# Kernel optimization log

Hardware: AMD Instinct MI355X
Metric: run time of the kernel (lower is better)

The kernel has to match this reference:

```python
import jax, jax.numpy as jnp
import numpy as np

N = 50000      # nodes
E = 800000     # edges
F_IN = 64      # num_node_features
H = 128        # hidden_channels
C = 2          # num_classes
G = 16         # graphs in batch


def setup_inputs() -> dict:
    key = jax.random.key(0)
    ks = jax.random.split(key, 16)
    def lin(k, fan_in, shape):
        return jax.random.normal(k, shape, jnp.float32) / np.sqrt(fan_in)
    return {
        "x": jax.random.normal(ks[0], (N, F_IN), jnp.float32),
        "edge_index": jax.random.randint(ks[1], (2, E), 0, N, dtype=jnp.int32),
        "batch": jnp.sort(jax.random.randint(ks[2], (N,), 0, G, dtype=jnp.int32)),
        "W1": lin(ks[3], F_IN, (F_IN, H)), "b1": jnp.zeros((H,), jnp.float32),
        "W2": lin(ks[4], H, (H, H)),       "b2": jnp.zeros((H,), jnp.float32),
        "W3": lin(ks[5], H, (H, H)),       "b3": jnp.zeros((H,), jnp.float32),
        "W4": lin(ks[6], H, (H, H)),       "b4": jnp.zeros((H,), jnp.float32),
        "lw1": lin(ks[7], H, (H, H // 2)), "lb1": jnp.zeros((H // 2,), jnp.float32),
        "lw2": lin(ks[8], H // 2, (H // 2, C)), "lb2": jnp.zeros((C,), jnp.float32),
    }


def _graph_norm(edge_index):
    # PyG GCNConv default: add self-loops, symmetric normalization.
    loop = jnp.arange(N, dtype=edge_index.dtype)
    src = jnp.concatenate([edge_index[0], loop])  # message source
    dst = jnp.concatenate([edge_index[1], loop])  # aggregation target
    deg = jax.ops.segment_sum(jnp.ones_like(dst, jnp.float32), dst, num_segments=N)
    dinv = jnp.where(deg > 0, jax.lax.rsqrt(deg), 0.0)
    norm = dinv[src] * dinv[dst]                  # [E+N]
    return src, dst, norm


def _gcn_conv(h, W, b, src, dst, norm):
    hw = h @ W                                    # [N, out]
    msg = hw[src] * norm[:, None]                 # gather + normalize  [E+N, out]
    agg = jax.ops.segment_sum(msg, dst, num_segments=N)  # scatter-add
    return agg + b


def reference(x, edge_index, batch, W1, b1, W2, b2, W3, b3, W4, b4, lw1, lb1, lw2, lb2):
    src, dst, norm = _graph_norm(edge_index)
    h = jax.nn.relu(_gcn_conv(x, W1, b1, src, dst, norm))   # dropout inactive (eval)
    h = jax.nn.relu(_gcn_conv(h, W2, b2, src, dst, norm))
    h = jax.nn.relu(_gcn_conv(h, W3, b3, src, dst, norm))
    h = _gcn_conv(h, W4, b4, src, dst, norm)
    # global_mean_pool over graph ids
    cnt = jax.ops.segment_sum(jnp.ones((N,), jnp.float32), batch, num_segments=G)
    pooled = jax.ops.segment_sum(h, batch, num_segments=G) / jnp.maximum(cnt, 1.0)[:, None]
    out = jax.nn.relu(pooled @ lw1 + lb1)
    return out @ lw2 + lb2
```

## Files before the change

### kernel.cpp

```cpp
#include <hip/hip_runtime.h>

#define NN 50000
#define NPAD 50048
#define NE 800000
#define FIN 64
#define H 128
#define NG 16
#define NPART 64
#define NBUCK 196
#define BUCK_CAP 4800
#define FILLA_BLOCKS 512
#define FILLA_CHUNK 1563
#define ROW_U 64
#define XROW_U 32
#define DUMMY NN
#define ZERO_I4 32768
#define PREP_ITEMS (H * FIN + 2 * H * H + ZERO_I4)
#define PREP_BLOCKS ((PREP_ITEMS + 255) / 256)

typedef __bf16 bf16x8 __attribute__((ext_vector_type(8)));
typedef float f32x4 __attribute__((ext_vector_type(4)));
typedef float f32x2 __attribute__((ext_vector_type(2)));
typedef unsigned int u32x4 __attribute__((ext_vector_type(4)));

__device__ inline unsigned short bf16r(float x) {
    unsigned int u = __float_as_uint(x);
    return (unsigned short)((u + 0x7fffu + ((u >> 16) & 1u)) >> 16);
}
__device__ inline unsigned int pack_bf16x2(float a, float b) {
    return (unsigned int)bf16r(a) | ((unsigned int)bf16r(b) << 16);
}
__device__ inline float bf_lo(unsigned int u) { return __uint_as_float(u << 16); }
__device__ inline float bf_hi(unsigned int u) { return __uint_as_float(u & 0xffff0000u); }

__device__ inline void pkadd(f32x2& a, unsigned int u) {
    f32x2 p;
    p.x = bf_lo(u);
    p.y = bf_hi(u);
    asm("v_pk_add_f32 %0, %1, %0" : "+v"(a) : "v"(p));
}
__device__ inline void bfly(f32x2& a, int m) {
    a.x += __shfl_xor(a.x, m);
    a.y += __shfl_xor(a.y, m);
}

__global__ __launch_bounds__(256) void fillA_prep_kernel(const int* __restrict__ ei,
                                                         int* __restrict__ gcount,
                                                         unsigned int* __restrict__ ebuf,
                                                         const float* __restrict__ W1,
                                                         const float* __restrict__ W2,
                                                         const float* __restrict__ W3,
                                                         unsigned short* __restrict__ Wt1,
                                                         unsigned short* __restrict__ Wt2,
                                                         unsigned short* __restrict__ Wt3,
                                                         int4* __restrict__ zbuf) {
    const int t = threadIdx.x;
    if (blockIdx.x >= FILLA_BLOCKS) {
        int e = (blockIdx.x - FILLA_BLOCKS) * 256 + t;
        if (e < H * FIN) {
            int n = e / FIN, k = e % FIN;
            Wt1[e] = bf16r(W1[k * H + n]);
            return;
        }
        int u = e - H * FIN;
        if (u < 2 * H * H) {
            const float* W = W2;
            unsigned short* Wt = Wt2;
            if (u >= H * H) { W = W3; Wt = Wt3; u -= H * H; }
            int n = u / H, k = u % H;
            Wt[u] = bf16r(W[k * H + n]);
            return;
        }
        int z = u - 2 * H * H;
        if (z < ZERO_I4) zbuf[z] = make_int4(0, 0, 0, 0);
        return;
    }
    __shared__ int hist[256];
    __shared__ int base[256];
    hist[t] = 0;
    __syncthreads();
    const int e0 = blockIdx.x * FILLA_CHUNK;
    const int e1 = min(e0 + FILLA_CHUNK, NE);
    for (int e = e0 + t; e < e1; e += 256)
        atomicAdd(&hist[ei[NE + e] >> 8], 1);
    __syncthreads();
    {
        int h = hist[t];
        base[t] = h ? atomicAdd(&gcount[t], h) : 0;
    }
    __syncthreads();
    for (int e = e0 + t; e < e1; e += 256) {
        int d = ei[NE + e];
        int s = ei[e];
        int b = d >> 8;
        int pos = atomicAdd(&base[b], 1);
        ebuf[b * BUCK_CAP + pos] = (unsigned int)s | ((unsigned int)d << 16);
    }
}

__global__ __launch_bounds__(256) void fillB_kernel(const unsigned int* __restrict__ ebuf,
                                                    const int* __restrict__ gcount,
                                                    int* __restrict__ galloc,
                                                    int* __restrict__ pcnt,
                                                    const int* __restrict__ batch,
                                                    int2* __restrict__ rowse,
                                                    float* __restrict__ dinv,
                                                    unsigned short* __restrict__ csr) {
    __shared__ int lh[256];
    __shared__ int lsum[256];
    __shared__ int lcur[256];
    __shared__ int lgc[16];
    __shared__ int base_s;
    const int b = blockIdx.x, t = threadIdx.x;
    const int n0 = b * 256;
    lh[t] = 0;
    if (t < 16) lgc[t] = 0;
    __syncthreads();
    const int ne = gcount[b];
    const unsigned int* __restrict__ eb = ebuf + b * BUCK_CAP;
    for (int i = t; i < ne; i += 256)
        atomicAdd(&lh[(int)(eb[i] >> 16) - n0], 1);
    __syncthreads();
    const int c = lh[t];
    const int p = (c + 7) & ~7;
    const int n = n0 + t;
    if (n < NN) atomicAdd(&lgc[batch[n]], 1);
    lsum[t] = p;
    __syncthreads();
    if (t < 16 && lgc[t]) atomicAdd(&pcnt[t], lgc[t]);
    for (int off = 1; off < 256; off <<= 1) {
        int u = (t >= off) ? lsum[t - off] : 0;
        __syncthreads();
        lsum[t] += u;
        __syncthreads();
    }
    if (t == 255) base_s = atomicAdd(galloc, lsum[255]);
    const int excl = t ? lsum[t - 1] : 0;
    __syncthreads();
    const int st = base_s + excl;
    if (n < NN) {
        rowse[n] = make_int2(st, st + p);
        dinv[n] = rsqrtf((float)c + 1.0f);
    } else if (n < NPAD) {
        rowse[n] = make_int2(0, 0);
        dinv[n] = 0.0f;
    }
    lcur[t] = st;
    __syncthreads();
    for (int i = t; i < ne; i += 256) {
        unsigned int u = eb[i];
        int pos = atomicAdd(&lcur[(int)(u >> 16) - n0], 1);
        csr[pos] = (unsigned short)(u & 0xFFFFu);
    }
    __syncthreads();
    for (int k = st + c; k < st + p; k++) csr[k] = (unsigned short)DUMMY;
}

__global__ __launch_bounds__(256) void xprep_kernel(const float* __restrict__ x,
                                                    const float* __restrict__ dinv,
                                                    unsigned short* __restrict__ xb) {
    const int idx = blockIdx.x * 256 + threadIdx.x;
    const int e4 = idx * 4;
    const int n = e4 >> 6;
    uint2 o;
    if (n < NN) {
        float4 v = *(const float4*)&x[e4];
        float d = dinv[n];
        o.x = pack_bf16x2(v.x * d, v.y * d);
        o.y = pack_bf16x2(v.z * d, v.w * d);
    } else {
        o.x = o.y = 0u;
    }
    *(uint2*)&xb[e4] = o;
}

#define LSTRIDE 130
template <int K, int EPI>
__global__ __launch_bounds__(256) void gemm_mfma_kernel(const unsigned short* __restrict__ hb,
                                                        const unsigned short* __restrict__ Wt,
                                                        const float* __restrict__ dinv,
                                                        const float* __restrict__ bias,
                                                        unsigned int* __restrict__ outu) {
    __shared__ float ls[64 * LSTRIDE];
    const int wave = threadIdx.x >> 6, lane = threadIdx.x & 63;
    const int m15 = lane & 15, quad = lane >> 4;
    const int row0 = blockIdx.x * 64;
    const int arow = row0 + wave * 16 + m15;

    bf16x8 a[K / 32];
#pragma unroll
    for (int ks = 0; ks < K / 32; ks++)
        a[ks] = *(const bf16x8*)&hb[(size_t)arow * K + ks * 32 + quad * 8];

    const int lrow = wave * 16 + quad * 4;
    float dv[4];
    if (EPI == 0) {
#pragma unroll
        for (int r = 0; r < 4; r++) dv[r] = dinv[row0 + lrow + r];
    }

#pragma unroll
    for (int ct = 0; ct < 8; ct++) {
        f32x4 acc = {0.f, 0.f, 0.f, 0.f};
#pragma unroll
        for (int ks = 0; ks < K / 32; ks++) {
            bf16x8 b = *(const bf16x8*)&Wt[(ct * 16 + m15) * K + ks * 32 + quad * 8];
            acc = __builtin_amdgcn_mfma_f32_16x16x32_bf16(a[ks], b, acc, 0, 0, 0);
        }
        float bv = (EPI == 1) ? bias[ct * 16 + m15] : 0.f;
#pragma unroll
        for (int r = 0; r < 4; r++) {
            float v = (EPI == 0) ? acc[r] * dv[r] : fmaxf(acc[r] + bv, 0.f);
            ls[(lrow + r) * LSTRIDE + ct * 16 + m15] = v;
        }
    }
    __syncthreads();

#pragma unroll
    for (int k = 0; k < 4; k++) {
        int idx = threadIdx.x + 256 * k;
        int row = idx >> 4, q = idx & 15;
        const float* p = &ls[row * LSTRIDE + q * 8];
        u32x4 o;
        o[0] = pack_bf16x2(p[0], p[1]);
        o[1] = pack_bf16x2(p[2], p[3]);
        o[2] = pack_bf16x2(p[4], p[5]);
        o[3] = pack_bf16x2(p[6], p[7]);
        if (EPI == 1 && row0 + row >= NN) { o[0] = o[1] = o[2] = o[3] = 0u; }
        __builtin_nontemporal_store(
            o, (u32x4*)&outu[(size_t)(row0 + row) * ROW_U + q * 4]);
    }
}

template <int RU>
__device__ inline void gather_row(const unsigned int* __restrict__ hwc,
                                  const int2* __restrict__ rowse,
                                  const unsigned short* __restrict__ csr,
                                  int n, int u0,
                                  f32x2& a0, f32x2& a1, f32x2& a2, f32x2& a3) {
    uint4 sv = *(const uint4*)&hwc[(size_t)n * RU + u0];
    a0.x = bf_lo(sv.x); a0.y = bf_hi(sv.x);
    a1.x = bf_lo(sv.y); a1.y = bf_hi(sv.y);
    a2.x = bf_lo(sv.z); a2.y = bf_hi(sv.z);
    a3.x = bf_lo(sv.w); a3.y = bf_hi(sv.w);
    const int2 se = rowse[n];
    int i = se.x;
    for (; i + 16 <= se.y; i += 16) {
        u32x4 c0 = __builtin_nontemporal_load((const u32x4*)&csr[i]);
        u32x4 c1 = __builtin_nontemporal_load((const u32x4*)&csr[i + 8]);
        int s0 = c0[0] & 0xFFFF, s1 = c0[0] >> 16;
        int s2 = c0[1] & 0xFFFF, s3 = c0[1] >> 16;
        int s4 = c0[2] & 0xFFFF, s5 = c0[2] >> 16;
        int s6 = c0[3] & 0xFFFF, s7 = c0[3] >> 16;
        int t0 = c1[0] & 0xFFFF, t1 = c1[0] >> 16;
        int t2 = c1[1] & 0xFFFF, t3 = c1[1] >> 16;
        int t4 = c1[2] & 0xFFFF, t5 = c1[2] >> 16;
        int t6 = c1[3] & 0xFFFF, t7 = c1[3] >> 16;
        uint4 v0 = *(const uint4*)&hwc[(size_t)s0 * RU + u0];
        uint4 v1 = *(const uint4*)&hwc[(size_t)s1 * RU + u0];
        uint4 v2 = *(const uint4*)&hwc[(size_t)s2 * RU + u0];
        uint4 v3 = *(const uint4*)&hwc[(size_t)s3 * RU + u0];
        uint4 v4 = *(const uint4*)&hwc[(size_t)s4 * RU + u0];
        uint4 v5 = *(const uint4*)&hwc[(size_t)s5 * RU + u0];
        uint4 v6 = *(const uint4*)&hwc[(size_t)s6 * RU + u0];
        uint4 v7 = *(const uint4*)&hwc[(size_t)s7 * RU + u0];
        uint4 w0 = *(const uint4*)&hwc[(size_t)t0 * RU + u0];
        uint4 w1 = *(const uint4*)&hwc[(size_t)t1 * RU + u0];
        uint4 w2 = *(const uint4*)&hwc[(size_t)t2 * RU + u0];
        uint4 w3 = *(const uint4*)&hwc[(size_t)t3 * RU + u0];
        uint4 w4 = *(const uint4*)&hwc[(size_t)t4 * RU + u0];
        uint4 w5 = *(const uint4*)&hwc[(size_t)t5 * RU + u0];
        uint4 w6 = *(const uint4*)&hwc[(size_t)t6 * RU + u0];
        uint4 w7 = *(const uint4*)&hwc[(size_t)t7 * RU + u0];
        pkadd(a0, v0.x); pkadd(a1, v0.y); pkadd(a2, v0.z); pkadd(a3, v0.w);
        pkadd(a0, v1.x); pkadd(a1, v1.y); pkadd(a2, v1.z); pkadd(a3, v1.w);
        pkadd(a0, v2.x); pkadd(a1, v2.y); pkadd(a2, v2.z); pkadd(a3, v2.w);
        pkadd(a0, v3.x); pkadd(a1, v3.y); pkadd(a2, v3.z); pkadd(a3, v3.w);
        pkadd(a0, v4.x); pkadd(a1, v4.y); pkadd(a2, v4.z); pkadd(a3, v4.w);
        pkadd(a0, v5.x); pkadd(a1, v5.y); pkadd(a2, v5.z); pkadd(a3, v5.w);
        pkadd(a0, v6.x); pkadd(a1, v6.y); pkadd(a2, v6.z); pkadd(a3, v6.w);
        pkadd(a0, v7.x); pkadd(a1, v7.y); pkadd(a2, v7.z); pkadd(a3, v7.w);
        pkadd(a0, w0.x); pkadd(a1, w0.y); pkadd(a2, w0.z); pkadd(a3, w0.w);
        pkadd(a0, w1.x); pkadd(a1, w1.y); pkadd(a2, w1.z); pkadd(a3, w1.w);
        pkadd(a0, w2.x); pkadd(a1, w2.y); pkadd(a2, w2.z); pkadd(a3, w2.w);
        pkadd(a0, w3.x); pkadd(a1, w3.y); pkadd(a2, w3.z); pkadd(a3, w3.w);
        pkadd(a0, w4.x); pkadd(a1, w4.y); pkadd(a2, w4.z); pkadd(a3, w4.w);
        pkadd(a0, w5.x); pkadd(a1, w5.y); pkadd(a2, w5.z); pkadd(a3, w5.w);
        pkadd(a0, w6.x); pkadd(a1, w6.y); pkadd(a2, w6.z); pkadd(a3, w6.w);
        pkadd(a0, w7.x); pkadd(a1, w7.y); pkadd(a2, w7.z); pkadd(a3, w7.w);
    }
    if (i < se.y) {
        u32x4 c = __builtin_nontemporal_load((const u32x4*)&csr[i]);
        int s0 = c[0] & 0xFFFF, s1 = c[0] >> 16;
        int s2 = c[1] & 0xFFFF, s3 = c[1] >> 16;
        int s4 = c[2] & 0xFFFF, s5 = c[2] >> 16;
        int s6 = c[3] & 0xFFFF, s7 = c[3] >> 16;
        uint4 v0 = *(const uint4*)&hwc[(size_t)s0 * RU + u0];
        uint4 v1 = *(const uint4*)&hwc[(size_t)s1 * RU + u0];
        uint4 v2 = *(const uint4*)&hwc[(size_t)s2 * RU + u0];
        uint4 v3 = *(const uint4*)&hwc[(size_t)s3 * RU + u0];
        uint4 v4 = *(const uint4*)&hwc[(size_t)s4 * RU + u0];
        uint4 v5 = *(const uint4*)&hwc[(size_t)s5 * RU + u0];
        uint4 v6 = *(const uint4*)&hwc[(size_t)s6 * RU + u0];
        uint4 v7 = *(const uint4*)&hwc[(size_t)s7 * RU + u0];
        pkadd(a0, v0.x); pkadd(a1, v0.y); pkadd(a2, v0.z); pkadd(a3, v0.w);
        pkadd(a0, v1.x); pkadd(a1, v1.y); pkadd(a2, v1.z); pkadd(a3, v1.w);
        pkadd(a0, v2.x); pkadd(a1, v2.y); pkadd(a2, v2.z); pkadd(a3, v2.w);
        pkadd(a0, v3.x); pkadd(a1, v3.y); pkadd(a2, v3.z); pkadd(a3, v3.w);
        pkadd(a0, v4.x); pkadd(a1, v4.y); pkadd(a2, v4.z); pkadd(a3, v4.w);
        pkadd(a0, v5.x); pkadd(a1, v5.y); pkadd(a2, v5.z); pkadd(a3, v5.w);
        pkadd(a0, v6.x); pkadd(a1, v6.y); pkadd(a2, v6.z); pkadd(a3, v6.w);
        pkadd(a0, v7.x); pkadd(a1, v7.y); pkadd(a2, v7.z); pkadd(a3, v7.w);
    }
}

__global__ __launch_bounds__(256) void aggx_kernel(const unsigned int* __restrict__ xbu,
                                                   const int2* __restrict__ rowse,
                                                   const unsigned short* __restrict__ csr,
                                                   const float* __restrict__ dinv,
                                                   unsigned int* __restrict__ xa) {
    const int u0 = (threadIdx.x & 7) * 4;
    const int n = blockIdx.x * 32 + (threadIdx.x >> 3);
    f32x2 a0, a1, a2, a3;
    gather_row<XROW_U>(xbu, rowse, csr, n, u0, a0, a1, a2, a3);
    const float d = dinv[n];
    u32x4 o;
    o[0] = pack_bf16x2(a0.x * d, a0.y * d);
    o[1] = pack_bf16x2(a1.x * d, a1.y * d);
    o[2] = pack_bf16x2(a2.x * d, a2.y * d);
    o[3] = pack_bf16x2(a3.x * d, a3.y * d);
    __builtin_nontemporal_store(o, (u32x4*)&xa[(size_t)n * XROW_U + u0]);
}

template <int MODE>
__global__ __launch_bounds__(256) void agg_kernel(const unsigned int* __restrict__ hwc,
                                                  const int2* __restrict__ rowse,
                                                  const unsigned short* __restrict__ csr,
                                                  const float* __restrict__ dinv,
                                                  const float* __restrict__ bias,
                                                  const int* __restrict__ batch,
                                                  float* __restrict__ poolpart,
                                                  unsigned int* __restrict__ outc) {
    const int u = threadIdx.x & 15;
    const int u0 = u * 4;
    if (MODE != 1) {
        const int n = blockIdx.x * 16 + (threadIdx.x >> 4);
        f32x2 a0, a1, a2, a3;
        gather_row<ROW_U>(hwc, rowse, csr, n, u0, a0, a1, a2, a3);
        const float d = dinv[n];
        const float2* bp = (const float2*)bias + u0;
        float2 q0 = bp[0], q1 = bp[1], q2 = bp[2], q3 = bp[3];
        float r0 = fmaxf(a0.x * d + q0.x, 0.f), r1 = fmaxf(a0.y * d + q0.y, 0.f);
        float r2 = fmaxf(a1.x * d + q1.x, 0.f), r3 = fmaxf(a1.y * d + q1.y, 0.f);
        float r4 = fmaxf(a2.x * d + q2.x, 0.f), r5 = fmaxf(a2.y * d + q2.y, 0.f);
        float r6 = fmaxf(a3.x * d + q3.x, 0.f), r7 = fmaxf(a3.y * d + q3.y, 0.f);
        if (MODE == 2) {
            r0 *= d; r1 *= d; r2 *= d; r3 *= d;
            r4 *= d; r5 *= d; r6 *= d; r7 *= d;
        }
        u32x4 o;
        o[0] = pack_bf16x2(r0, r1);
        o[1] = pack_bf16x2(r2, r3);
        o[2] = pack_bf16x2(r4, r5);
        o[3] = pack_bf16x2(r6, r7);
        __builtin_nontemporal_store(o, (u32x4*)&outc[(size_t)n * ROW_U + u0]);
        return;
    }
    __shared__ float lds[4][128];
    const int nip = threadIdx.x >> 4;
    const int lane = threadIdx.x & 63, wave = threadIdx.x >> 6;
    const int n0 = blockIdx.x * 64;
    const int copy = blockIdx.x & (NPART - 1);
    const int gfirst0 = batch[n0];
    const bool blockUni = (gfirst0 == batch[min(n0 + 63, NN - 1)]);
    float* __restrict__ ppb = poolpart + copy * (NG * H);
    f32x2 acc0 = {0.f, 0.f}, acc1 = {0.f, 0.f}, acc2 = {0.f, 0.f}, acc3 = {0.f, 0.f};
#pragma unroll
    for (int p = 0; p < 4; p++) {
        const int n = n0 + p * 16 + nip;
        f32x2 t0, t1, t2, t3;
        gather_row<ROW_U>(hwc, rowse, csr, n, u0, t0, t1, t2, t3);
        const float d = dinv[n];
        t0 *= d; t1 *= d; t2 *= d; t3 *= d;
        if (blockUni) {
            acc0 += t0; acc1 += t1; acc2 += t2; acc3 += t3;
        } else {
            const int gb = batch[min(n, NN - 1)];
            const bool uni = (__shfl(gb, 0) == __shfl(gb, 63));
            if (uni) {
                bfly(t0, 16); bfly(t1, 16); bfly(t2, 16); bfly(t3, 16);
                bfly(t0, 32); bfly(t1, 32); bfly(t2, 32); bfly(t3, 32);
                if (lane < 16) {
                    float* q = ppb + __shfl(gb, 0) * H + lane * 8;
                    atomicAdd(&q[0], t0.x); atomicAdd(&q[1], t0.y);
                    atomicAdd(&q[2], t1.x); atomicAdd(&q[3], t1.y);
                    atomicAdd(&q[4], t2.x); atomicAdd(&q[5], t2.y);
                    atomicAdd(&q[6], t3.x); atomicAdd(&q[7], t3.y);
                }
            } else if (n < NN) {
                float* q = ppb + gb * H + u * 8;
                atomicAdd(&q[0], t0.x); atomicAdd(&q[1], t0.y);
                atomicAdd(&q[2], t1.x); atomicAdd(&q[3], t1.y);
                atomicAdd(&q[4], t2.x); atomicAdd(&q[5], t2.y);
                atomicAdd(&q[6], t3.x); atomicAdd(&q[7], t3.y);
            }
        }
    }
    if (blockUni) {
        bfly(acc0, 16); bfly(acc1, 16); bfly(acc2, 16); bfly(acc3, 16);
        bfly(acc0, 32); bfly(acc1, 32); bfly(acc2, 32); bfly(acc3, 32);
        if (lane < 16) {
            float* q = &lds[wave][lane * 8];
            q[0] = acc0.x; q[1] = acc0.y;
            q[2] = acc1.x; q[3] = acc1.y;
            q[4] = acc2.x; q[5] = acc2.y;
            q[6] = acc3.x; q[7] = acc3.y;
        }
        __syncthreads();
        if (threadIdx.x < 128) {
            float tot = lds[0][threadIdx.x] + lds[1][threadIdx.x] +
                        lds[2][threadIdx.x] + lds[3][threadIdx.x];
            atomicAdd(&ppb[gfirst0 * H + threadIdx.x], tot);
        }
    }
}

__global__ __launch_bounds__(1024) void mlp_kernel(const float* __restrict__ poolpart,
                                                   const int* __restrict__ pcnt,
                                                   const float* __restrict__ W4,
                                                   const float* __restrict__ b4,
                                                   const float* __restrict__ lw1,
                                                   const float* __restrict__ lb1,
                                                   const float* __restrict__ lw2,
                                                   const float* __restrict__ lb2,
                                                   float* __restrict__ out) {
    __shared__ float mean_s[NG * H];
    __shared__ float z_s[NG * H];
    __shared__ float cnt_s[NG];
    __shared__ float hid_s[NG * 64];
    int tid = threadIdx.x;
    if (tid < NG) cnt_s[tid] = fmaxf((float)pcnt[tid], 1.0f);
    __syncthreads();
    for (int i = tid; i < NG * H; i += 1024) {
        float s = 0.f;
        for (int p = 0; p < NPART; p++) s += poolpart[p * (NG * H) + i];
        mean_s[i] = s / cnt_s[i >> 7];
    }
    __syncthreads();
#pragma unroll
    for (int r = 0; r < 2; r++) {
        int i = tid + r * 1024;
        int g = i >> 7, j = i & (H - 1);
        float acc = b4[j];
        for (int f = 0; f < H; f++) acc += mean_s[g * H + f] * W4[f * H + j];
        z_s[i] = acc;
    }
    __syncthreads();
    {
        int g = tid >> 6, j = tid & 63;
        float acc = lb1[j];
        for (int f = 0; f < H; f++) acc += z_s[g * H + f] * lw1[f * 64 + j];
        hid_s[g * 64 + j] = fmaxf(acc, 0.f);
    }
    __syncthreads();
    if (tid < 32) {
        int g = tid >> 1, c = tid & 1;
        float acc = lb2[c];
        for (int j = 0; j < 64; j++) acc += hid_s[g * 64 + j] * lw2[j * 2 + c];
        out[g * 2 + c] = acc;
    }
}

extern "C" void kernel_launch(void* const* d_in, const int* in_sizes, int n_in,
                              void* d_out, int out_size, void* d_ws, size_t ws_size,
                              hipStream_t stream) {
    const float* x = (const float*)d_in[0];
    const int* ei = (const int*)d_in[1];
    const int* batch = (const int*)d_in[2];
    const float* W1 = (const float*)d_in[3];
    const float* b1 = (const float*)d_in[4];
    const float* W2 = (const float*)d_in[5];
    const float* b2 = (const float*)d_in[6];
    const float* W3 = (const float*)d_in[7];
    const float* b3 = (const float*)d_in[8];
    const float* W4 = (const float*)d_in[9];
    const float* b4 = (const float*)d_in[10];
    const float* lw1 = (const float*)d_in[11];
    const float* lb1 = (const float*)d_in[12];
    const float* lw2 = (const float*)d_in[13];
    const float* lb2 = (const float*)d_in[14];
    float* out = (float*)d_out;

    int* wsi = (int*)d_ws;
    int* gcount = wsi;
    int* galloc = wsi + 256;
    int* pcnt = wsi + 280;
    float* poolpart = (float*)(wsi + 512);
    int2* rowse = (int2*)(wsi + 131584);
    unsigned short* csr = (unsigned short*)(wsi + 231680);
    float* dinv = (float*)(wsi + 831680);
    unsigned short* Wt1 = (unsigned short*)(wsi + 881728);
    unsigned short* Wt2 = (unsigned short*)(wsi + 885824);
    unsigned short* Wt3 = (unsigned short*)(wsi + 894016);
    unsigned short* xb = (unsigned short*)(wsi + 910400);
    unsigned int* hb = (unsigned int*)(wsi + 2511936);
    unsigned int* hwb = (unsigned int*)(wsi + 5715008);
    unsigned int* ebuf = (unsigned int*)(wsi + 8918080);

    const int gemmBlocks = NPAD / 64;
    const int xprepBlocks = NPAD * FIN / 1024;
    const int aggxBlocks = NPAD / 32;
    const int agg0Blocks = NPAD / 16;
    const int poolBlocks = NPAD / 64;

    hipMemsetAsync(wsi, 0, 512 * sizeof(int), stream);
    fillA_prep_kernel<<<FILLA_BLOCKS + PREP_BLOCKS, 256, 0, stream>>>(
        ei, gcount, ebuf, W1, W2, W3, Wt1, Wt2, Wt3, (int4*)poolpart);
    fillB_kernel<<<NBUCK, 256, 0, stream>>>(ebuf, gcount, galloc, pcnt, batch,
                                            rowse, dinv, csr);

    xprep_kernel<<<xprepBlocks, 256, 0, stream>>>(x, dinv, xb);
    aggx_kernel<<<aggxBlocks, 256, 0, stream>>>((const unsigned int*)xb, rowse, csr,
                                                dinv, hwb);
    gemm_mfma_kernel<FIN, 1><<<gemmBlocks, 256, 0, stream>>>((unsigned short*)hwb, Wt1,
                                                             nullptr, b1, hb);
    gemm_mfma_kernel<H, 0><<<gemmBlocks, 256, 0, stream>>>((unsigned short*)hb, Wt2,
                                                           dinv, nullptr, hwb);
    agg_kernel<0><<<agg0Blocks, 256, 0, stream>>>(hwb, rowse, csr, dinv, b2, batch,
                                                  nullptr, hb);
    gemm_mfma_kernel<H, 0><<<gemmBlocks, 256, 0, stream>>>((unsigned short*)hb, Wt3,
                                                           dinv, nullptr, hwb);
    agg_kernel<2><<<agg0Blocks, 256, 0, stream>>>(hwb, rowse, csr, dinv, b3, batch,
                                                  nullptr, hb);
    agg_kernel<1><<<poolBlocks, 256, 0, stream>>>(hb, rowse, csr, dinv, nullptr, batch,
                                                  poolpart, nullptr);

    mlp_kernel<<<1, 1024, 0, stream>>>(poolpart, pcnt, W4, b4, lw1, lb1, lw2, lb2, out);
}
```

Baseline: 291.1 us.

## Fuse x prep into fillB and fuse aggregation gathers into GEMM kernels

Moves the x scaling and bf16 conversion into fillB_kernel, computing dinv from the per-block histogram. The first-layer gather now feeds gemm1f through shared memory, and the layer-2 gather plus bias and relu feeds the layer-3 GEMM in gemm3f. This removes three launches and the global round trips of intermediate activations. In exchange the fused kernels use more shared memory and have longer, irregular gather phases that may reduce occupancy. Buffer ping-pong roles between hb and hwb are swapped to match.

```diff
diff --git a/kernel.cpp b/kernel.cpp
--- a/kernel.cpp
+++ b/kernel.cpp
@@ -103,8 +103,10 @@
                                                     int* __restrict__ galloc,
                                                     int* __restrict__ pcnt,
                                                     const int* __restrict__ batch,
+                                                    const float* __restrict__ x,
                                                     int2* __restrict__ rowse,
                                                     float* __restrict__ dinv,
+                                                    unsigned short* __restrict__ xb,
                                                     unsigned short* __restrict__ csr) {
     __shared__ int lh[256];
     __shared__ int lsum[256];
@@ -154,81 +156,18 @@
     }
     __syncthreads();
     for (int k = st + c; k < st + p; k++) csr[k] = (unsigned short)DUMMY;
-}
-
-__global__ __launch_bounds__(256) void xprep_kernel(const float* __restrict__ x,
-                                                    const float* __restrict__ dinv,
-                                                    unsigned short* __restrict__ xb) {
-    const int idx = blockIdx.x * 256 + threadIdx.x;
-    const int e4 = idx * 4;
-    const int n = e4 >> 6;
-    uint2 o;
-    if (n < NN) {
-        float4 v = *(const float4*)&x[e4];
-        float d = dinv[n];
-        o.x = pack_bf16x2(v.x * d, v.y * d);
-        o.y = pack_bf16x2(v.z * d, v.w * d);
-    } else {
-        o.x = o.y = 0u;
-    }
-    *(uint2*)&xb[e4] = o;
-}
-
-#define LSTRIDE 130
-template <int K, int EPI>
-__global__ __launch_bounds__(256) void gemm_mfma_kernel(const unsigned short* __restrict__ hb,
-                                                        const unsigned short* __restrict__ Wt,
-                                                        const float* __restrict__ dinv,
-                                                        const float* __restrict__ bias,
-                                                        unsigned int* __restrict__ outu) {
-    __shared__ float ls[64 * LSTRIDE];
-    const int wave = threadIdx.x >> 6, lane = threadIdx.x & 63;
-    const int m15 = lane & 15, quad = lane >> 4;
-    const int row0 = blockIdx.x * 64;
-    const int arow = row0 + wave * 16 + m15;
-
-    bf16x8 a[K / 32];
-#pragma unroll
-    for (int ks = 0; ks < K / 32; ks++)
-        a[ks] = *(const bf16x8*)&hb[(size_t)arow * K + ks * 32 + quad * 8];
-
-    const int lrow = wave * 16 + quad * 4;
-    float dv[4];
-    if (EPI == 0) {
-#pragma unroll
-        for (int r = 0; r < 4; r++) dv[r] = dinv[row0 + lrow + r];
-    }
-
-#pragma unroll
-    for (int ct = 0; ct < 8; ct++) {
-        f32x4 acc = {0.f, 0.f, 0.f, 0.f};
-#pragma unroll
-        for (int ks = 0; ks < K / 32; ks++) {
-            bf16x8 b = *(const bf16x8*)&Wt[(ct * 16 + m15) * K + ks * 32 + quad * 8];
-            acc = __builtin_amdgcn_mfma_f32_16x16x32_bf16(a[ks], b, acc, 0, 0, 0);
-        }
-        float bv = (EPI == 1) ? bias[ct * 16 + m15] : 0.f;
-#pragma unroll
-        for (int r = 0; r < 4; r++) {
-            float v = (EPI == 0) ? acc[r] * dv[r] : fmaxf(acc[r] + bv, 0.f);
-            ls[(lrow + r) * LSTRIDE + ct * 16 + m15] = v;
-        }
-    }
-    __syncthreads();
-
-#pragma unroll
-    for (int k = 0; k < 4; k++) {
-        int idx = threadIdx.x + 256 * k;
-        int row = idx >> 4, q = idx & 15;
-        const float* p = &ls[row * LSTRIDE + q * 8];
-        u32x4 o;
-        o[0] = pack_bf16x2(p[0], p[1]);
-        o[1] = pack_bf16x2(p[2], p[3]);
-        o[2] = pack_bf16x2(p[4], p[5]);
-        o[3] = pack_bf16x2(p[6], p[7]);
-        if (EPI == 1 && row0 + row >= NN) { o[0] = o[1] = o[2] = o[3] = 0u; }
-        __builtin_nontemporal_store(
-            o, (u32x4*)&outu[(size_t)(row0 + row) * ROW_U + q * 4]);
+    for (int i = t; i < 4096; i += 256) {
+        int nl = i >> 4;
+        int nn = n0 + nl;
+        if (nn >= NPAD) continue;
+        uint2 o = make_uint2(0u, 0u);
+        if (nn < NN) {
+            float4 v = *(const float4*)&x[(size_t)nn * 64 + (i & 15) * 4];
+            float d = rsqrtf((float)lh[nl] + 1.0f);
+            o.x = pack_bf16x2(v.x * d, v.y * d);
+            o.y = pack_bf16x2(v.z * d, v.w * d);
+        }
+        *(uint2*)&xb[(size_t)nn * 64 + (i & 15) * 4] = o;
     }
 }
 
@@ -314,22 +253,198 @@
     }
 }
 
-__global__ __launch_bounds__(256) void aggx_kernel(const unsigned int* __restrict__ xbu,
-                                                   const int2* __restrict__ rowse,
-                                                   const unsigned short* __restrict__ csr,
-                                                   const float* __restrict__ dinv,
-                                                   unsigned int* __restrict__ xa) {
-    const int u0 = (threadIdx.x & 7) * 4;
-    const int n = blockIdx.x * 32 + (threadIdx.x >> 3);
-    f32x2 a0, a1, a2, a3;
-    gather_row<XROW_U>(xbu, rowse, csr, n, u0, a0, a1, a2, a3);
-    const float d = dinv[n];
-    u32x4 o;
-    o[0] = pack_bf16x2(a0.x * d, a0.y * d);
-    o[1] = pack_bf16x2(a1.x * d, a1.y * d);
-    o[2] = pack_bf16x2(a2.x * d, a2.y * d);
-    o[3] = pack_bf16x2(a3.x * d, a3.y * d);
-    __builtin_nontemporal_store(o, (u32x4*)&xa[(size_t)n * XROW_U + u0]);
+#define LSTRIDE 130
+
+__global__ __launch_bounds__(256) void gemm1f_kernel(const unsigned short* __restrict__ xb,
+                                                     const int2* __restrict__ rowse,
+                                                     const unsigned short* __restrict__ csr,
+                                                     const float* __restrict__ dinv,
+                                                     const unsigned short* __restrict__ Wt,
+                                                     const float* __restrict__ bias,
+                                                     unsigned int* __restrict__ outu) {
+    __shared__ unsigned int als[64 * 36];
+    __shared__ float ls[64 * LSTRIDE];
+    const int wave = threadIdx.x >> 6, lane = threadIdx.x & 63;
+    const int m15 = lane & 15, quad = lane >> 4;
+    const int row0 = blockIdx.x * 64;
+
+    {
+        const int u0 = (threadIdx.x & 7) * 4;
+#pragma unroll
+        for (int p = 0; p < 2; p++) {
+            const int nl = p * 32 + (threadIdx.x >> 3);
+            const int n = row0 + nl;
+            f32x2 a0, a1, a2, a3;
+            gather_row<XROW_U>((const unsigned int*)xb, rowse, csr, n, u0, a0, a1, a2, a3);
+            const float d = dinv[n];
+            u32x4 o;
+            o[0] = pack_bf16x2(a0.x * d, a0.y * d);
+            o[1] = pack_bf16x2(a1.x * d, a1.y * d);
+            o[2] = pack_bf16x2(a2.x * d, a2.y * d);
+            o[3] = pack_bf16x2(a3.x * d, a3.y * d);
+            *(u32x4*)&als[nl * 36 + (threadIdx.x & 7) * 4] = o;
+        }
+    }
+    __syncthreads();
+
+    bf16x8 a[2];
+#pragma unroll
+    for (int ks = 0; ks < 2; ks++)
+        a[ks] = *(const bf16x8*)&als[(wave * 16 + m15) * 36 + ks * 16 + quad * 4];
+
+    const int lrow = wave * 16 + quad * 4;
+#pragma unroll
+    for (int ct = 0; ct < 8; ct++) {
+        f32x4 acc = {0.f, 0.f, 0.f, 0.f};
+#pragma unroll
+        for (int ks = 0; ks < 2; ks++) {
+            bf16x8 bfr = *(const bf16x8*)&Wt[(ct * 16 + m15) * FIN + ks * 32 + quad * 8];
+            acc = __builtin_amdgcn_mfma_f32_16x16x32_bf16(a[ks], bfr, acc, 0, 0, 0);
+        }
+        float bv = bias[ct * 16 + m15];
+#pragma unroll
+        for (int r = 0; r < 4; r++)
+            ls[(lrow + r) * LSTRIDE + ct * 16 + m15] = fmaxf(acc[r] + bv, 0.f);
+    }
+    __syncthreads();
+
+#pragma unroll
+    for (int k = 0; k < 4; k++) {
+        int idx = threadIdx.x + 256 * k;
+        int row = idx >> 4, q = idx & 15;
+        const float* p = &ls[row * LSTRIDE + q * 8];
+        u32x4 o;
+        o[0] = pack_bf16x2(p[0], p[1]);
+        o[1] = pack_bf16x2(p[2], p[3]);
+        o[2] = pack_bf16x2(p[4], p[5]);
+        o[3] = pack_bf16x2(p[6], p[7]);
+        if (row0 + row >= NN) { o[0] = o[1] = o[2] = o[3] = 0u; }
+        __builtin_nontemporal_store(
+            o, (u32x4*)&outu[(size_t)(row0 + row) * ROW_U + q * 4]);
+    }
+}
+
+__global__ __launch_bounds__(256) void gemm2_kernel(const unsigned short* __restrict__ hb,
+                                                    const unsigned short* __restrict__ Wt,
+                                                    const float* __restrict__ dinv,
+                                                    unsigned int* __restrict__ outu) {
+    __shared__ float ls[64 * LSTRIDE];
+    const int wave = threadIdx.x >> 6, lane = threadIdx.x & 63;
+    const int m15 = lane & 15, quad = lane >> 4;
+    const int row0 = blockIdx.x * 64;
+    const int arow = row0 + wave * 16 + m15;
+
+    bf16x8 a[4];
+#pragma unroll
+    for (int ks = 0; ks < 4; ks++)
+        a[ks] = *(const bf16x8*)&hb[(size_t)arow * H + ks * 32 + quad * 8];
+
+    const int lrow = wave * 16 + quad * 4;
+    float dv[4];
+#pragma unroll
+    for (int r = 0; r < 4; r++) dv[r] = dinv[row0 + lrow + r];
+
+#pragma unroll
+    for (int ct = 0; ct < 8; ct++) {
+        f32x4 acc = {0.f, 0.f, 0.f, 0.f};
+#pragma unroll
+        for (int ks = 0; ks < 4; ks++) {
+            bf16x8 bfr = *(const bf16x8*)&Wt[(ct * 16 + m15) * H + ks * 32 + quad * 8];
+            acc = __builtin_amdgcn_mfma_f32_16x16x32_bf16(a[ks], bfr, acc, 0, 0, 0);
+        }
+#pragma unroll
+        for (int r = 0; r < 4; r++)
+            ls[(lrow + r) * LSTRIDE + ct * 16 + m15] = acc[r] * dv[r];
+    }
+    __syncthreads();
+
+#pragma unroll
+    for (int k = 0; k < 4; k++) {
+        int idx = threadIdx.x + 256 * k;
+        int row = idx >> 4, q = idx & 15;
+        const float* p = &ls[row * LSTRIDE + q * 8];
+        u32x4 o;
+        o[0] = pack_bf16x2(p[0], p[1]);
+        o[1] = pack_bf16x2(p[2], p[3]);
+        o[2] = pack_bf16x2(p[4], p[5]);
+        o[3] = pack_bf16x2(p[6], p[7]);
+        __builtin_nontemporal_store(
+            o, (u32x4*)&outu[(size_t)(row0 + row) * ROW_U + q * 4]);
+    }
+}
+
+__global__ __launch_bounds__(256) void gemm3f_kernel(const unsigned int* __restrict__ hwc,
+                                                     const int2* __restrict__ rowse,
+                                                     const unsigned short* __restrict__ csr,
+                                                     const float* __restrict__ dinv,
+                                                     const float* __restrict__ bias,
+                                                     const unsigned short* __restrict__ Wt,
+                                                     unsigned int* __restrict__ outu) {
+    __shared__ unsigned int als[64 * 68];
+    __shared__ float ls[64 * LSTRIDE];
+    const int wave = threadIdx.x >> 6, lane = threadIdx.x & 63;
+    const int m15 = lane & 15, quad = lane >> 4;
+    const int row0 = blockIdx.x * 64;
+
+    {
+        const int u = threadIdx.x & 15;
+        const int u0 = u * 4;
+        const float2* bp = (const float2*)bias + u0;
+        float2 q0 = bp[0], q1 = bp[1], q2 = bp[2], q3 = bp[3];
+#pragma unroll
+        for (int p = 0; p < 4; p++) {
+            const int nl = p * 16 + (threadIdx.x >> 4);
+            const int n = row0 + nl;
+            f32x2 a0, a1, a2, a3;
+            gather_row<ROW_U>(hwc, rowse, csr, n, u0, a0, a1, a2, a3);
+            const float d = dinv[n];
+            u32x4 o;
+            o[0] = pack_bf16x2(fmaxf(a0.x * d + q0.x, 0.f), fmaxf(a0.y * d + q0.y, 0.f));
+            o[1] = pack_bf16x2(fmaxf(a1.x * d + q1.x, 0.f), fmaxf(a1.y * d + q1.y, 0.f));
+            o[2] = pack_bf16x2(fmaxf(a2.x * d + q2.x, 0.f), fmaxf(a2.y * d + q2.y, 0.f));
+            o[3] = pack_bf16x2(fmaxf(a3.x * d + q3.x, 0.f), fmaxf(a3.y * d + q3.y, 0.f));
+            *(u32x4*)&als[nl * 68 + u0] = o;
+        }
+    }
+    __syncthreads();
+
+    bf16x8 a[4];
+#pragma unroll
+    for (int ks = 0; ks < 4; ks++)
+        a[ks] = *(const bf16x8*)&als[(wave * 16 + m15) * 68 + ks * 16 + quad * 4];
+
+    const int lrow = wave * 16 + quad * 4;
+    float dv[4];
+#pragma unroll
+    for (int r = 0; r < 4; r++) dv[r] = dinv[row0 + lrow + r];
+
+#pragma unroll
+    for (int ct = 0; ct < 8; ct++) {
+        f32x4 acc = {0.f, 0.f, 0.f, 0.f};
+#pragma unroll
+        for (int ks = 0; ks < 4; ks++) {
+            bf16x8 bfr = *(const bf16x8*)&Wt[(ct * 16 + m15) * H + ks * 32 + quad * 8];
+            acc = __builtin_amdgcn_mfma_f32_16x16x32_bf16(a[ks], bfr, acc, 0, 0, 0);
+        }
+#pragma unroll
+        for (int r = 0; r < 4; r++)
+            ls[(lrow + r) * LSTRIDE + ct * 16 + m15] = acc[r] * dv[r];
+    }
+    __syncthreads();
+
+#pragma unroll
+    for (int k = 0; k < 4; k++) {
+        int idx = threadIdx.x + 256 * k;
+        int row = idx >> 4, q = idx & 15;
+        const float* p = &ls[row * LSTRIDE + q * 8];
+        u32x4 o;
+        o[0] = pack_bf16x2(p[0], p[1]);
+        o[1] = pack_bf16x2(p[2], p[3]);
+        o[2] = pack_bf16x2(p[4], p[5]);
+        o[3] = pack_bf16x2(p[6], p[7]);
+        __builtin_nontemporal_store(
+            o, (u32x4*)&outu[(size_t)(row0 + row) * ROW_U + q * 4]);
+    }
 }
 
 template <int MODE>
@@ -508,31 +623,21 @@
     unsigned int* ebuf = (unsigned int*)(wsi + 8918080);
 
     const int gemmBlocks = NPAD / 64;
-    const int xprepBlocks = NPAD * FIN / 1024;
-    const int aggxBlocks = NPAD / 32;
     const int agg0Blocks = NPAD / 16;
     const int poolBlocks = NPAD / 64;
 
     hipMemsetAsync(wsi, 0, 512 * sizeof(int), stream);
     fillA_prep_kernel<<<FILLA_BLOCKS + PREP_BLOCKS, 256, 0, stream>>>(
         ei, gcount, ebuf, W1, W2, W3, Wt1, Wt2, Wt3, (int4*)poolpart);
-    fillB_kernel<<<NBUCK, 256, 0, stream>>>(ebuf, gcount, galloc, pcnt, batch,
-                                            rowse, dinv, csr);
-
-    xprep_kernel<<<xprepBlocks, 256, 0, stream>>>(x, dinv, xb);
-    aggx_kernel<<<aggxBlocks, 256, 0, stream>>>((const unsigned int*)xb, rowse, csr,
-                                                dinv, hwb);
-    gemm_mfma_kernel<FIN, 1><<<gemmBlocks, 256, 0, stream>>>((unsigned short*)hwb, Wt1,
-                                                             nullptr, b1, hb);
-    gemm_mfma_kernel<H, 0><<<gemmBlocks, 256, 0, stream>>>((unsigned short*)hb, Wt2,
-                                                           dinv, nullptr, hwb);
-    agg_kernel<0><<<agg0Blocks, 256, 0, stream>>>(hwb, rowse, csr, dinv, b2, batch,
-                                                  nullptr, hb);
-    gemm_mfma_kernel<H, 0><<<gemmBlocks, 256, 0, stream>>>((unsigned short*)hb, Wt3,
-                                                           dinv, nullptr, hwb);
-    agg_kernel<2><<<agg0Blocks, 256, 0, stream>>>(hwb, rowse, csr, dinv, b3, batch,
-                                                  nullptr, hb);
-    agg_kernel<1><<<poolBlocks, 256, 0, stream>>>(hb, rowse, csr, dinv, nullptr, batch,
+    fillB_kernel<<<NBUCK, 256, 0, stream>>>(ebuf, gcount, galloc, pcnt, batch, x,
+                                            rowse, dinv, xb, csr);
+
+    gemm1f_kernel<<<gemmBlocks, 256, 0, stream>>>(xb, rowse, csr, dinv, Wt1, b1, hb);
+    gemm2_kernel<<<gemmBlocks, 256, 0, stream>>>((unsigned short*)hb, Wt2, dinv, hwb);
+    gemm3f_kernel<<<gemmBlocks, 256, 0, stream>>>(hwb, rowse, csr, dinv, b2, Wt3, hb);
+    agg_kernel<2><<<agg0Blocks, 256, 0, stream>>>(hb, rowse, csr, dinv, b3, batch,
+                                                  nullptr, hwb);
+    agg_kernel<1><<<poolBlocks, 256, 0, stream>>>(hwb, rowse, csr, dinv, nullptr, batch,
                                                   poolpart, nullptr);
 
     mlp_kernel<<<1, 1024, 0, stream>>>(poolpart, pcnt, W4, b4, lw1, lb1, lw2, lb2, out);
```

Result: slower. 298.0 us (+2.4%).
